# Kernel tuning notes

Measured on AMD Instinct MI355X. Metric: run time of the kernel, lower is better.

Reference implementation:

```python
import jax, jax.numpy as jnp
import numpy as np
from jax import lax

RATIOS = [0.5, 1.0, 2.0]
SCALES = [8, 16, 32]
BASE = 16
FEAT_STRIDE = 16
NMS_THRESH = 0.7
PRE_NMS = 2000
POST_NMS = 300
MIN_SIZE = 16.0
SCALE = 1.0
A = len(RATIOS) * len(SCALES)  # 9


def _anchor_base():
    ab = []
    py = px = BASE / 2.0
    for r in RATIOS:
        for s in SCALES:
            h = BASE * s * np.sqrt(r)
            w = BASE * s * np.sqrt(1.0 / r)
            ab.append([py - h / 2.0, px - w / 2.0, py + h / 2.0, px + w / 2.0])
    return jnp.asarray(np.array(ab, dtype=np.float32))  # (A,4)


def _shifted_anchors(H, W):
    base = _anchor_base()
    sy = jnp.arange(H, dtype=jnp.float32) * FEAT_STRIDE
    sx = jnp.arange(W, dtype=jnp.float32) * FEAT_STRIDE
    gy, gx = jnp.meshgrid(sy, sx, indexing='ij')
    shift = jnp.stack([gy.ravel(), gx.ravel(), gy.ravel(), gx.ravel()], axis=1)  # (K,4)
    return (shift[:, None, :] + base[None, :, :]).reshape(-1, 4)  # (K*A,4)


def _conv(x, w, b, pad):
    y = lax.conv_general_dilated(x, w, (1, 1), ((pad, pad), (pad, pad)),
                                 dimension_numbers=('NCHW', 'OIHW', 'NCHW'))
    return y + b[None, :, None, None]


def _loc2bbox(anchor, loc):
    h = anchor[:, 2] - anchor[:, 0]
    w = anchor[:, 3] - anchor[:, 1]
    cy = anchor[:, 0] + 0.5 * h
    cx = anchor[:, 1] + 0.5 * w
    dy, dx, dh, dw = loc[:, 0], loc[:, 1], loc[:, 2], loc[:, 3]
    ncy = dy * h + cy
    ncx = dx * w + cx
    nh = jnp.exp(dh) * h
    nw = jnp.exp(dw) * w
    return jnp.stack([ncy - 0.5 * nh, ncx - 0.5 * nw, ncy + 0.5 * nh, ncx + 0.5 * nw], axis=1)


def _iou_matrix(b):
    area = (b[:, 2] - b[:, 0]) * (b[:, 3] - b[:, 1])
    ty = jnp.maximum(b[:, None, 0], b[None, :, 0])
    tx = jnp.maximum(b[:, None, 1], b[None, :, 1])
    by = jnp.minimum(b[:, None, 2], b[None, :, 2])
    bx = jnp.minimum(b[:, None, 3], b[None, :, 3])
    inter = jnp.maximum(by - ty, 0.0) * jnp.maximum(bx - tx, 0.0)
    return inter / (area[:, None] + area[None, :] - inter)


def _proposals(loc_i, fg_i, anchor, img_h, img_w):
    boxes = _loc2bbox(anchor, loc_i)
    boxes = jnp.stack([
        jnp.clip(boxes[:, 0], 0.0, float(img_h)),
        jnp.clip(boxes[:, 1], 0.0, float(img_w)),
        jnp.clip(boxes[:, 2], 0.0, float(img_h)),
        jnp.clip(boxes[:, 3], 0.0, float(img_w)),
    ], axis=1)
    hs = boxes[:, 2] - boxes[:, 0]
    ws = boxes[:, 3] - boxes[:, 1]
    valid = (hs >= MIN_SIZE * SCALE) & (ws >= MIN_SIZE * SCALE)
    sc = jnp.where(valid, fg_i, -jnp.inf)
    top_sc, idx = lax.top_k(sc, PRE_NMS)          # sorted by score desc
    b = boxes[idx]                                # (PRE_NMS,4)
    iou = _iou_matrix(b)                          # (PRE_NMS,PRE_NMS)
    rng = jnp.arange(PRE_NMS)

    def body(i, keep):
        sup = (iou[i] > NMS_THRESH) & keep[i] & (rng > i)
        return keep & ~sup

    keep = lax.fori_loop(0, PRE_NMS, body, top_sc > -jnp.inf)
    order = jnp.argsort(jnp.where(keep, rng, PRE_NMS))  # kept indices first, score order
    sel = order[:POST_NMS]
    n_keep = jnp.sum(keep)
    valid_out = jnp.arange(POST_NMS) < n_keep
    rois = jnp.where(valid_out[:, None], b[sel], 0.0)
    return rois, valid_out


def setup_inputs() -> dict:
    key = jax.random.key(0)
    ks = jax.random.split(key, 4)
    return {
        'x': jax.random.normal(ks[0], (4, 1024, 64, 64), dtype=jnp.float32),
        'conv1_w': 0.01 * jax.random.normal(ks[1], (512, 1024, 3, 3), dtype=jnp.float32),
        'conv1_b': jnp.zeros((512,), dtype=jnp.float32),
        'score_w': 0.01 * jax.random.normal(ks[2], (18, 512, 1, 1), dtype=jnp.float32),
        'score_b': jnp.zeros((18,), dtype=jnp.float32),
        'loc_w': 0.01 * jax.random.normal(ks[3], (36, 512, 1, 1), dtype=jnp.float32),
        'loc_b': jnp.zeros((36,), dtype=jnp.float32),
        'img_h': 1024,
        'img_w': 1024,
    }


def reference(x, conv1_w, conv1_b, score_w, score_b, loc_w, loc_b, img_h, img_w):
    n, _, H, W = x.shape
    anchor = _shifted_anchors(H, W)                       # (HWA,4)
    mid = jax.nn.relu(_conv(x, conv1_w, conv1_b, 1))
    rpn_locs = _conv(mid, loc_w, loc_b, 0).transpose(0, 2, 3, 1).reshape(n, -1, 4)
    rpn_scores = _conv(mid, score_w, score_b, 0).transpose(0, 2, 3, 1)
    soft = jax.nn.softmax(rpn_scores.reshape(n, H, W, A, 2), axis=4)
    rpn_fg = soft[..., 1].reshape(n, -1)
    rpn_scores = rpn_scores.reshape(n, -1, 2)
    rois, valid = jax.vmap(lambda l, s: _proposals(l, s, anchor, img_h, img_w))(rpn_locs, rpn_fg)
    roi_indices = jnp.where(valid, jnp.arange(n, dtype=jnp.int32)[:, None], -1)
    return (rpn_locs, rpn_scores, rois.reshape(-1, 4), roi_indices.reshape(-1), anchor)
```

## Files before the change

### kernel.cpp

```cpp
#include <hip/hip_runtime.h>
#include <math.h>

#define NIMG 4
#define CIN 1024
#define CMID 512
#define HGT 64
#define WID 64
#define NA 9
#define NPOS 36864
#define PRE 2000
#define POST 300

#define LOCOFF   0
#define SCOREOFF 589824
#define ROISOFF  884736
#define RIDXOFF  889536
#define ANCHOFF  890736

__global__ __launch_bounds__(256) void wtrans_kernel(
    const float* __restrict__ w, float* __restrict__ wt)
{
    __shared__ float ts[64][65];
    const int t = threadIdx.x;
    const int rt0 = blockIdx.x * 64;
    const int ct0 = blockIdx.y * 64;
    const int j = t & 63;
    const int i0 = t >> 6;
#pragma unroll
    for (int k = 0; k < 16; ++k) {
        int i = i0 + k * 4;
        ts[i][j] = w[(size_t)(ct0 + i) * (CIN * 9) + rt0 + j];
    }
    __syncthreads();
#pragma unroll
    for (int k = 0; k < 16; ++k) {
        int jj = i0 + k * 4;
        wt[(size_t)(rt0 + jj) * CMID + ct0 + j] = ts[j][jj];
    }
}

__global__ __launch_bounds__(256) void conv1_kernel(
    const float* __restrict__ x, const float* __restrict__ wt,
    const float* __restrict__ bias, float* __restrict__ mid)
{
    __shared__ __align__(16) double xs[4][6][68];
    __shared__ __align__(16) double wsh[4][9][32];
    const int t = threadIdx.x;
    const int rowgrp = blockIdx.x, coutgrp = blockIdx.y, img = blockIdx.z;
    const int r0 = rowgrp * 4, c0 = coutgrp * 32;
    const int pixgrp = t & 7, cgrp = (t >> 3) & 7, rowi = t >> 6;
    const int p0 = pixgrp * 8, cc0 = cgrp * 4;

    double acc[8][4];
#pragma unroll
    for (int i = 0; i < 8; ++i)
#pragma unroll
        for (int c = 0; c < 4; ++c) acc[i][c] = 0.0;

    for (int ci0 = 0; ci0 < CIN; ci0 += 4) {
        for (int idx = t; idx < 4 * 6 * 66; idx += 256) {
            int cin = idx / 396, rem = idx % 396;
            int row = rem / 66, col = rem % 66;
            int gr = r0 - 1 + row, gc = col - 1;
            float v = 0.f;
            if (gr >= 0 && gr < HGT && gc >= 0 && gc < WID)
                v = x[((img * CIN + ci0 + cin) * HGT + gr) * WID + gc];
            xs[cin][row][col] = (double)v;
        }
        for (int idx = t; idx < 4 * 9 * 32; idx += 256) {
            int cout = idx & 31, r = idx >> 5;
            wsh[r / 9][r % 9][cout] =
                (double)wt[(size_t)((ci0 + r / 9) * 9 + r % 9) * CMID + c0 + cout];
        }
        __syncthreads();

#pragma unroll 1
        for (int cin = 0; cin < 4; ++cin) {
#pragma unroll
            for (int dy = 0; dy < 3; ++dy) {
                const double* xr = &xs[cin][rowi + dy][p0];
                double2 a0 = *(const double2*)(xr);
                double2 a1 = *(const double2*)(xr + 2);
                double2 a2 = *(const double2*)(xr + 4);
                double2 a3 = *(const double2*)(xr + 6);
                double2 a4 = *(const double2*)(xr + 8);
                double xd[10];
                xd[0] = a0.x; xd[1] = a0.y; xd[2] = a1.x; xd[3] = a1.y;
                xd[4] = a2.x; xd[5] = a2.y; xd[6] = a3.x; xd[7] = a3.y;
                xd[8] = a4.x; xd[9] = a4.y;
#pragma unroll
                for (int dx = 0; dx < 3; ++dx) {
                    const double* wp = &wsh[cin][dy * 3 + dx][cc0];
                    double2 wa = *(const double2*)(wp);
                    double2 wb = *(const double2*)(wp + 2);
#pragma unroll
                    for (int i = 0; i < 8; ++i) {
                        double xv = xd[i + dx];
                        acc[i][0] += xv * wa.x;
                        acc[i][1] += xv * wa.y;
                        acc[i][2] += xv * wb.x;
                        acc[i][3] += xv * wb.y;
                    }
                }
            }
        }
        __syncthreads();
    }

#pragma unroll
    for (int co = 0; co < 4; ++co) {
        double bb = (double)bias[c0 + cc0 + co];
        float tmp[8];
#pragma unroll
        for (int i = 0; i < 8; ++i) {
            double v = acc[i][co] + bb;
            v = v > 0.0 ? v : 0.0;
            tmp[i] = (float)v;
        }
        float* dst = &mid[((img * CMID + c0 + cc0 + co) * HGT + (r0 + rowi)) * WID + p0];
        *(float4*)dst = make_float4(tmp[0], tmp[1], tmp[2], tmp[3]);
        *(float4*)(dst + 4) = make_float4(tmp[4], tmp[5], tmp[6], tmp[7]);
    }
}

__global__ __launch_bounds__(256) void conv1x1_kernel(
    const float* __restrict__ mid,
    const float* __restrict__ sw, const float* __restrict__ sb,
    const float* __restrict__ lw, const float* __restrict__ lb,
    float* __restrict__ out, double* __restrict__ locws, double* __restrict__ keyws)
{
    const int t = threadIdx.x;
    const int p = blockIdx.x * 256 + t;
    const int g = blockIdx.y;
    const int img = blockIdx.z;

    double acc[14];
#pragma unroll
    for (int k = 0; k < 14; ++k) acc[k] = 0.0;

    const float* mp = &mid[(size_t)img * CMID * 4096 + p];
    for (int cin = 0; cin < CMID; ++cin) {
        double xd = (double)mp[(size_t)cin * 4096];
#pragma unroll
        for (int k = 0; k < 14; ++k) {
            int c = g * 14 + k;
            double wv = 0.0;
            if (c < 36)      wv = (double)lw[c * CMID + cin];
            else if (c < 54) wv = (double)sw[(c - 36) * CMID + cin];
            acc[k] += xd * wv;
        }
    }

    double prev = 0.0;
#pragma unroll
    for (int k = 0; k < 14; ++k) {
        int c = g * 14 + k;
        if (c >= 54) continue;
        if (c < 36) {
            double v = acc[k] + (double)lb[c];
            int a = c >> 2, cc = c & 3;
            size_t ix = (size_t)img * NPOS + (size_t)p * NA + a;
            locws[ix * 4 + cc] = v;
            out[LOCOFF + ix * 4 + cc] = (float)v;
        } else {
            int sc = c - 36;
            double v = acc[k] + (double)sb[sc];
            int a = sc >> 1;
            size_t ix = (size_t)img * NPOS + (size_t)p * NA + a;
            out[SCOREOFF + ix * 2 + (sc & 1)] = (float)v;
            if (sc & 1) keyws[ix] = v - prev;
            prev = v;
        }
    }
}

__device__ __forceinline__ unsigned mono_of(double k) {
    unsigned fb = __float_as_uint((float)k);
    return (fb & 0x80000000u) ? ~fb : (fb | 0x80000000u);
}

__global__ __launch_bounds__(256) void boxes_kernel(
    double* __restrict__ keyio, const double* __restrict__ locws,
    const int* __restrict__ imh, const int* __restrict__ imw,
    float* __restrict__ out, double* __restrict__ boxes, unsigned* __restrict__ hist)
{
    __shared__ unsigned lh[4096];
    const int t = threadIdx.x;
    const int img = blockIdx.y;
    const int pos = blockIdx.x * 256 + t;
    for (int i = t; i < 4096; i += 256) lh[i] = 0;
    __syncthreads();

    int a = pos % 9, hw = pos / 9;
    int hy = hw >> 6, hx = hw & 63;
    int r_idx = a / 3, s_idx = a % 3;
    double ratio = r_idx == 0 ? 0.5 : (r_idx == 1 ? 1.0 : 2.0);
    double scl   = s_idx == 0 ? 8.0 : (s_idx == 1 ? 16.0 : 32.0);
    double hh2 = 8.0 * scl * sqrt(ratio);
    double ww2 = 8.0 * scl * sqrt(1.0 / ratio);
    float ay1 = (float)(8.0 - hh2), ax1 = (float)(8.0 - ww2);
    float ay2 = (float)(8.0 + hh2), ax2 = (float)(8.0 + ww2);
    float sy = (float)(hy * 16), sx = (float)(hx * 16);
    float A0 = sy + ay1, A1 = sx + ax1, A2 = sy + ay2, A3 = sx + ax2;
    if (img == 0) {
        size_t ao = ANCHOFF + (size_t)pos * 4;
        out[ao + 0] = A0; out[ao + 1] = A1; out[ao + 2] = A2; out[ao + 3] = A3;
    }

    size_t ix = (size_t)img * NPOS + pos;
    const double* lp = &locws[ix * 4];
    double h = (double)A2 - (double)A0, w_ = (double)A3 - (double)A1;
    double cy = (double)A0 + 0.5 * h, cx = (double)A1 + 0.5 * w_;
    double dy = lp[0], dx = lp[1], dh = lp[2], dw = lp[3];
    double ncy = dy * h + cy, ncx = dx * w_ + cx;
    double nh = exp(dh) * h, nw = exp(dw) * w_;
    double Hc = (double)imh[0], Wc = (double)imw[0];
    double y1 = ncy - 0.5 * nh, x1 = ncx - 0.5 * nw;
    double y2 = ncy + 0.5 * nh, x2 = ncx + 0.5 * nw;
    y1 = fmin(fmax(y1, 0.0), Hc); x1 = fmin(fmax(x1, 0.0), Wc);
    y2 = fmin(fmax(y2, 0.0), Hc); x2 = fmin(fmax(x2, 0.0), Wc);
    boxes[ix * 4 + 0] = y1; boxes[ix * 4 + 1] = x1;
    boxes[ix * 4 + 2] = y2; boxes[ix * 4 + 3] = x2;

    bool valid = ((y2 - y1) >= 16.0) && ((x2 - x1) >= 16.0);
    double kg = valid ? keyio[ix] : -INFINITY;
    keyio[ix] = kg;
    atomicAdd(&lh[mono_of(kg) >> 20], 1u);
    __syncthreads();
    for (int i = t; i < 4096; i += 256)
        if (lh[i]) atomicAdd(&hist[img * 4096 + i], lh[i]);
}

__global__ void cutoff_kernel(const unsigned* __restrict__ hist, int* __restrict__ cutoffb)
{
    if (threadIdx.x) return;
    int img = blockIdx.x;
    unsigned cum = 0; int cb = 0;
    for (int b = 4095; b >= 0; --b) {
        cum += hist[img * 4096 + b];
        if (cum >= PRE) { cb = b; break; }
    }
    cutoffb[img] = cb;
}

__global__ __launch_bounds__(256) void compact_kernel(
    const double* __restrict__ keyio, const int* __restrict__ cutoffb,
    int* __restrict__ candCnt, int* __restrict__ candIdx, double* __restrict__ candKey)
{
    int img = blockIdx.y;
    int pos = blockIdx.x * 256 + threadIdx.x;
    size_t ix = (size_t)img * NPOS + pos;
    double k = keyio[ix];
    if ((int)(mono_of(k) >> 20) >= cutoffb[img]) {
        int p = atomicAdd(&candCnt[img], 1);
        candIdx[img * NPOS + p] = pos;
        candKey[(size_t)img * NPOS + p] = k;
    }
}

__global__ __launch_bounds__(256) void rank_kernel(
    const int* __restrict__ candCnt, const int* __restrict__ candIdx,
    const double* __restrict__ candKey, const double* __restrict__ boxes,
    int* __restrict__ topIdx, int* __restrict__ topValid, double* __restrict__ bsel)
{
    __shared__ double sk[256];
    __shared__ int si[256];
    int img = blockIdx.y, t = threadIdx.x;
    int M = candCnt[img];
    if (blockIdx.x * 256 >= M) return;
    int i = blockIdx.x * 256 + t;
    bool act = i < M;
    double ki = 0.0; int pi = 0;
    if (act) { ki = candKey[(size_t)img * NPOS + i]; pi = candIdx[img * NPOS + i]; }
    int rank = 0;
    for (int jb = 0; jb < M; jb += 256) {
        int j = jb + t;
        if (j < M) { sk[t] = candKey[(size_t)img * NPOS + j]; si[t] = candIdx[img * NPOS + j]; }
        __syncthreads();
        int lim = min(256, M - jb);
        if (act) {
            for (int jj = 0; jj < lim; ++jj) {
                double kj = sk[jj]; int pj = si[jj];
                rank += (kj > ki || (kj == ki && pj < pi)) ? 1 : 0;
            }
        }
        __syncthreads();
    }
    if (act && rank < PRE) {
        topIdx[img * PRE + rank] = pi;
        topValid[img * PRE + rank] = (ki != -INFINITY) ? 1 : 0;
        const double* bp = &boxes[((size_t)img * NPOS + pi) * 4];
        double* bs = &bsel[((size_t)img * PRE + rank) * 4];
        bs[0] = bp[0]; bs[1] = bp[1]; bs[2] = bp[2]; bs[3] = bp[3];
    }
}

__global__ __launch_bounds__(256) void mask_kernel(
    const double* __restrict__ bsel, unsigned long long* __restrict__ mask)
{
    int i = blockIdx.x, img = blockIdx.y, t = threadIdx.x;
    const double* bi = &bsel[((size_t)img * PRE + i) * 4];
    double y1i = bi[0], x1i = bi[1], y2i = bi[2], x2i = bi[3];
    double ai = (y2i - y1i) * (x2i - x1i);
#pragma unroll 1
    for (int it = 0; it < 8; ++it) {
        int j = it * 256 + t;
        bool pred = false;
        if (j < PRE && j > i) {
            const double* bj = &bsel[((size_t)img * PRE + j) * 4];
            double ty = fmax(y1i, bj[0]), tx = fmax(x1i, bj[1]);
            double by = fmin(y2i, bj[2]), bx = fmin(x2i, bj[3]);
            double inter = fmax(by - ty, 0.0) * fmax(bx - tx, 0.0);
            double aj = (bj[2] - bj[0]) * (bj[3] - bj[1]);
            double iou = inter / (ai + aj - inter);
            pred = iou > 0.7;
        }
        unsigned long long m = __ballot(pred);
        if ((t & 63) == 0)
            mask[((size_t)img * PRE + i) * 32 + it * 4 + (t >> 6)] = m;
    }
}

__global__ void nms_kernel(const unsigned long long* __restrict__ mask,
                           const int* __restrict__ topValid, int* __restrict__ keepA)
{
    int img = blockIdx.x, lane = threadIdx.x;
    size_t base = (size_t)img * PRE;
    unsigned long long remv = 0;
    if (lane < 32) {
        unsigned long long tv = 0;
        for (int b = 0; b < 64; ++b) {
            int idx = lane * 64 + b;
            if (idx < PRE && topValid[base + idx]) tv |= (1ull << b);
        }
        remv = ~tv;
    }
    const unsigned long long* mrow = &mask[base * 32];
    unsigned long long c0 = 0, c1 = 0, c2 = 0, c3 = 0;
    if (lane < 32) {
        c0 = mrow[(size_t)0 * 32 + lane]; c1 = mrow[(size_t)1 * 32 + lane];
        c2 = mrow[(size_t)2 * 32 + lane]; c3 = mrow[(size_t)3 * 32 + lane];
    }
    for (int i = 0; i < PRE; i += 4) {
        unsigned long long n0 = 0, n1 = 0, n2 = 0, n3 = 0;
        if (lane < 32 && i + 4 < PRE) {
            n0 = mrow[(size_t)(i + 4) * 32 + lane];
            n1 = mrow[(size_t)(i + 5) * 32 + lane];
            n2 = mrow[(size_t)(i + 6) * 32 + lane];
            n3 = mrow[(size_t)(i + 7) * 32 + lane];
        }
        {
            unsigned long long rw = __shfl(remv, i >> 6);
            int kp = !((rw >> (i & 63)) & 1ull);
            if (lane == 0) keepA[base + i] = kp;
            if (kp) remv |= c0;
        }
        {
            int ii = i + 1;
            unsigned long long rw = __shfl(remv, ii >> 6);
            int kp = !((rw >> (ii & 63)) & 1ull);
            if (lane == 0) keepA[base + ii] = kp;
            if (kp) remv |= c1;
        }
        {
            int ii = i + 2;
            unsigned long long rw = __shfl(remv, ii >> 6);
            int kp = !((rw >> (ii & 63)) & 1ull);
            if (lane == 0) keepA[base + ii] = kp;
            if (kp) remv |= c2;
        }
        {
            int ii = i + 3;
            unsigned long long rw = __shfl(remv, ii >> 6);
            int kp = !((rw >> (ii & 63)) & 1ull);
            if (lane == 0) keepA[base + ii] = kp;
            if (kp) remv |= c3;
        }
        c0 = n0; c1 = n1; c2 = n2; c3 = n3;
    }
}

__global__ __launch_bounds__(256) void final_kernel(
    const int* __restrict__ keepA, const double* __restrict__ bsel, float* __restrict__ out)
{
    __shared__ int ssum[256];
    __shared__ int stot;
    int img = blockIdx.x, t = threadIdx.x;
    size_t base = (size_t)img * PRE;
    int loc[8]; int s = 0;
#pragma unroll
    for (int k = 0; k < 8; ++k) {
        int i = t * 8 + k;
        loc[k] = (i < PRE) ? keepA[base + i] : 0;
        s += loc[k];
    }
    ssum[t] = s;
    __syncthreads();
    if (t == 0) {
        int run = 0;
        for (int u = 0; u < 256; ++u) { int tmp = ssum[u]; ssum[u] = run; run += tmp; }
        stot = run;
    }
    __syncthreads();
    int run = ssum[t];
#pragma unroll
    for (int k = 0; k < 8; ++k) {
        int i = t * 8 + k;
        if (i < PRE && loc[k]) {
            int p = run++;
            if (p < POST) {
                const double* bp = &bsel[(base + i) * 4];
                size_t ro = ROISOFF + ((size_t)img * POST + p) * 4;
                out[ro + 0] = (float)bp[0]; out[ro + 1] = (float)bp[1];
                out[ro + 2] = (float)bp[2]; out[ro + 3] = (float)bp[3];
                out[RIDXOFF + img * POST + p] = (float)img;
            }
        }
    }
    __syncthreads();
    int nk = stot;
    for (int r = t; r < POST; r += 256) {
        if (r >= nk) {
            size_t ro = ROISOFF + ((size_t)img * POST + r) * 4;
            out[ro + 0] = 0.f; out[ro + 1] = 0.f; out[ro + 2] = 0.f; out[ro + 3] = 0.f;
            out[RIDXOFF + img * POST + r] = -1.f;
        }
    }
}

extern "C" void kernel_launch(void* const* d_in, const int* in_sizes, int n_in,
                              void* d_out, int out_size, void* d_ws, size_t ws_size,
                              hipStream_t stream)
{
    const float* x   = (const float*)d_in[0];
    const float* c1w = (const float*)d_in[1];
    const float* c1b = (const float*)d_in[2];
    const float* sw  = (const float*)d_in[3];
    const float* sb  = (const float*)d_in[4];
    const float* lw  = (const float*)d_in[5];
    const float* lb  = (const float*)d_in[6];
    const int*   ih  = (const int*)d_in[7];
    const int*   iw  = (const int*)d_in[8];
    float* out = (float*)d_out;
    (void)in_sizes; (void)n_in; (void)out_size; (void)ws_size;

    char* ws = (char*)d_ws;
    size_t off = 0;
    auto alloc = [&](size_t bytes) -> void* {
        void* p = (void*)(ws + off);
        off = (off + bytes + 255) & ~(size_t)255;
        return p;
    };
    float*  mid      = (float*) alloc((size_t)NIMG * CMID * 4096 * 4);
    float*  wtr      = (float*) alloc((size_t)CMID * CIN * 9 * 4);
    double* locws    = (double*)alloc((size_t)NIMG * NPOS * 4 * 8);
    double* keyws    = (double*)alloc((size_t)NIMG * NPOS * 8);
    double* boxes    = (double*)alloc((size_t)NIMG * NPOS * 4 * 8);
    unsigned* hist   = (unsigned*)alloc((size_t)NIMG * 4096 * 4);
    int*    cutoffb  = (int*)   alloc(64);
    int*    candCnt  = (int*)   alloc(64);
    int*    candIdx  = (int*)   alloc((size_t)NIMG * NPOS * 4);
    double* candKey  = (double*)alloc((size_t)NIMG * NPOS * 8);
    int*    topIdx   = (int*)   alloc((size_t)NIMG * PRE * 4);
    int*    topValid = (int*)   alloc((size_t)NIMG * PRE * 4);
    double* bsel     = (double*)alloc((size_t)NIMG * PRE * 4 * 8);
    unsigned long long* mask = (unsigned long long*)alloc((size_t)NIMG * PRE * 32 * 8);
    int*    keepA    = (int*)   alloc((size_t)NIMG * PRE * 4);

    hipMemsetAsync(hist, 0, (size_t)NIMG * 4096 * 4, stream);
    hipMemsetAsync(candCnt, 0, 64, stream);

    wtrans_kernel <<<dim3(144, 8),       256, 0, stream>>>(c1w, wtr);
    conv1_kernel  <<<dim3(16, 16, NIMG), 256, 0, stream>>>(x, wtr, c1b, mid);
    conv1x1_kernel<<<dim3(16, 4, NIMG),  256, 0, stream>>>(mid, sw, sb, lw, lb, out, locws, keyws);
    boxes_kernel  <<<dim3(144, NIMG),    256, 0, stream>>>(keyws, locws, ih, iw, out, boxes, hist);
    cutoff_kernel <<<NIMG, 64, 0, stream>>>(hist, cutoffb);
    compact_kernel<<<dim3(144, NIMG),    256, 0, stream>>>(keyws, cutoffb, candCnt, candIdx, candKey);
    rank_kernel   <<<dim3(144, NIMG),    256, 0, stream>>>(candCnt, candIdx, candKey, boxes,
                                                           topIdx, topValid, bsel);
    mask_kernel   <<<dim3(PRE, NIMG),    256, 0, stream>>>(bsel, mask);
    nms_kernel    <<<NIMG, 64, 0, stream>>>(mask, topValid, keepA);
    final_kernel  <<<NIMG, 256, 0, stream>>>(keepA, bsel, out);
}
```

Before: 4.748 ms.

## Retile FP64 conv1 to two rows per thread with register-prefetched input

The 3x3 conv kernel now gives each thread two output rows, so each loaded input row and weight value is reused across both rows and adjacent dy taps. Input staging doubles to 8 channels per step and is kept as float in LDS, converted to double on read. The next chunk is prefetched from global memory into registers while the current one computes. It also sets a minimum of 2 blocks per SM and halves the grid. The cost is more registers (64 double accumulators plus 21 prefetch floats), which could cause spills or lower occupancy, and fewer blocks (512) to fill the GPU.

```diff
diff --git a/kernel.cpp b/kernel.cpp
--- a/kernel.cpp
+++ b/kernel.cpp
@@ -39,87 +39,123 @@
     }
 }
 
-__global__ __launch_bounds__(256) void conv1_kernel(
+#define NXS (8 * 10 * 66)
+#define XPRE 21
+
+__global__ __launch_bounds__(256, 2) void conv1_kernel(
     const float* __restrict__ x, const float* __restrict__ wt,
     const float* __restrict__ bias, float* __restrict__ mid)
 {
-    __shared__ __align__(16) double xs[4][6][68];
-    __shared__ __align__(16) double wsh[4][9][32];
+    __shared__ float  Xl[8][10][67];
+    __shared__ double Wl[8][9][32];
     const int t = threadIdx.x;
-    const int rowgrp = blockIdx.x, coutgrp = blockIdx.y, img = blockIdx.z;
-    const int r0 = rowgrp * 4, c0 = coutgrp * 32;
-    const int pixgrp = t & 7, cgrp = (t >> 3) & 7, rowi = t >> 6;
-    const int p0 = pixgrp * 8, cc0 = cgrp * 4;
-
-    double acc[8][4];
-#pragma unroll
-    for (int i = 0; i < 8; ++i)
-#pragma unroll
-        for (int c = 0; c < 4; ++c) acc[i][c] = 0.0;
-
-    for (int ci0 = 0; ci0 < CIN; ci0 += 4) {
-        for (int idx = t; idx < 4 * 6 * 66; idx += 256) {
-            int cin = idx / 396, rem = idx % 396;
-            int row = rem / 66, col = rem % 66;
-            int gr = r0 - 1 + row, gc = col - 1;
-            float v = 0.f;
-            if (gr >= 0 && gr < HGT && gc >= 0 && gc < WID)
-                v = x[((img * CIN + ci0 + cin) * HGT + gr) * WID + gc];
-            xs[cin][row][col] = (double)v;
-        }
-        for (int idx = t; idx < 4 * 9 * 32; idx += 256) {
-            int cout = idx & 31, r = idx >> 5;
-            wsh[r / 9][r % 9][cout] =
-                (double)wt[(size_t)((ci0 + r / 9) * 9 + r % 9) * CMID + c0 + cout];
+    const int rowblk = blockIdx.x, coutblk = blockIdx.y, img = blockIdx.z;
+    const int y0 = rowblk * 8, cout0 = coutblk * 32;
+    const int pg = t & 7, cg = (t >> 3) & 7, rp = t >> 6;
+    const int p0 = pg * 8, cc0 = cg * 4, rp2 = rp * 2;
+
+    double acc[2][8][4];
+#pragma unroll
+    for (int rr = 0; rr < 2; ++rr)
+#pragma unroll
+        for (int i = 0; i < 8; ++i)
+#pragma unroll
+            for (int c = 0; c < 4; ++c) acc[rr][i][c] = 0.0;
+
+    float xpre[XPRE];
+
+#define XLOAD(CI0)                                                        \
+    {                                                                     \
+        _Pragma("unroll")                                                 \
+        for (int k = 0; k < XPRE; ++k) {                                  \
+            int idx = t + k * 256;                                        \
+            float v = 0.f;                                                \
+            if (idx < NXS) {                                              \
+                int cin = idx / 660, rem = idx % 660;                     \
+                int row = rem / 66, col = rem % 66;                       \
+                int gr = y0 - 1 + row, gc = col - 1;                      \
+                if (gr >= 0 && gr < HGT && gc >= 0 && gc < WID)           \
+                    v = x[((img * CIN + (CI0) + cin) * HGT + gr) * WID + gc]; \
+            }                                                             \
+            xpre[k] = v;                                                  \
+        }                                                                 \
+    }
+
+    XLOAD(0)
+
+#pragma unroll 1
+    for (int s = 0; s < 128; ++s) {
+        const int ci0 = s * 8;
+#pragma unroll
+        for (int k = 0; k < XPRE; ++k) {
+            int idx = t + k * 256;
+            if (idx < NXS) {
+                int cin = idx / 660, rem = idx % 660;
+                int row = rem / 66, col = rem % 66;
+                Xl[cin][row][col] = xpre[k];
+            }
+        }
+#pragma unroll
+        for (int k = 0; k < 9; ++k) {
+            int idx = t + k * 256;
+            int r = idx >> 5, cl = idx & 31;
+            Wl[r / 9][r % 9][cl] =
+                (double)wt[(size_t)((ci0 + r / 9) * 9 + (r % 9)) * CMID + cout0 + cl];
         }
         __syncthreads();
 
+        if (s + 1 < 128) XLOAD(ci0 + 8)
+
+#define LOADROW(DST, CIN, LROW)                                           \
+        _Pragma("unroll")                                                 \
+        for (int j = 0; j < 10; ++j)                                      \
+            DST[j] = (double)Xl[CIN][LROW][p0 + j];
+
+#define TAP(CIN, DY, RA, RB)                                              \
+        _Pragma("unroll")                                                 \
+        for (int dx = 0; dx < 3; ++dx) {                                  \
+            const double* wp = &Wl[CIN][(DY) * 3 + dx][cc0];              \
+            double w0 = wp[0], w1 = wp[1], w2 = wp[2], w3 = wp[3];        \
+            _Pragma("unroll")                                             \
+            for (int i = 0; i < 8; ++i) {                                 \
+                double xa = RA[i + dx], xb = RB[i + dx];                  \
+                acc[0][i][0] += xa * w0; acc[0][i][1] += xa * w1;         \
+                acc[0][i][2] += xa * w2; acc[0][i][3] += xa * w3;         \
+                acc[1][i][0] += xb * w0; acc[1][i][1] += xb * w1;         \
+                acc[1][i][2] += xb * w2; acc[1][i][3] += xb * w3;         \
+            }                                                             \
+        }
+
 #pragma unroll 1
-        for (int cin = 0; cin < 4; ++cin) {
-#pragma unroll
-            for (int dy = 0; dy < 3; ++dy) {
-                const double* xr = &xs[cin][rowi + dy][p0];
-                double2 a0 = *(const double2*)(xr);
-                double2 a1 = *(const double2*)(xr + 2);
-                double2 a2 = *(const double2*)(xr + 4);
-                double2 a3 = *(const double2*)(xr + 6);
-                double2 a4 = *(const double2*)(xr + 8);
-                double xd[10];
-                xd[0] = a0.x; xd[1] = a0.y; xd[2] = a1.x; xd[3] = a1.y;
-                xd[4] = a2.x; xd[5] = a2.y; xd[6] = a3.x; xd[7] = a3.y;
-                xd[8] = a4.x; xd[9] = a4.y;
-#pragma unroll
-                for (int dx = 0; dx < 3; ++dx) {
-                    const double* wp = &wsh[cin][dy * 3 + dx][cc0];
-                    double2 wa = *(const double2*)(wp);
-                    double2 wb = *(const double2*)(wp + 2);
-#pragma unroll
-                    for (int i = 0; i < 8; ++i) {
-                        double xv = xd[i + dx];
-                        acc[i][0] += xv * wa.x;
-                        acc[i][1] += xv * wa.y;
-                        acc[i][2] += xv * wb.x;
-                        acc[i][3] += xv * wb.y;
-                    }
-                }
+        for (int cin = 0; cin < 8; ++cin) {
+            double r0d[10], r1d[10], r2d[10], r3d[10];
+            LOADROW(r0d, cin, rp2 + 0)
+            LOADROW(r1d, cin, rp2 + 1)
+            TAP(cin, 0, r0d, r1d)
+            LOADROW(r2d, cin, rp2 + 2)
+            TAP(cin, 1, r1d, r2d)
+            LOADROW(r3d, cin, rp2 + 3)
+            TAP(cin, 2, r2d, r3d)
+        }
+        __syncthreads();
+    }
+
+#pragma unroll
+    for (int rr = 0; rr < 2; ++rr) {
+#pragma unroll
+        for (int co = 0; co < 4; ++co) {
+            double bb = (double)bias[cout0 + cc0 + co];
+            float tmp[8];
+#pragma unroll
+            for (int i = 0; i < 8; ++i) {
+                double v = acc[rr][i][co] + bb;
+                v = v > 0.0 ? v : 0.0;
+                tmp[i] = (float)v;
             }
-        }
-        __syncthreads();
-    }
-
-#pragma unroll
-    for (int co = 0; co < 4; ++co) {
-        double bb = (double)bias[c0 + cc0 + co];
-        float tmp[8];
-#pragma unroll
-        for (int i = 0; i < 8; ++i) {
-            double v = acc[i][co] + bb;
-            v = v > 0.0 ? v : 0.0;
-            tmp[i] = (float)v;
-        }
-        float* dst = &mid[((img * CMID + c0 + cc0 + co) * HGT + (r0 + rowi)) * WID + p0];
-        *(float4*)dst = make_float4(tmp[0], tmp[1], tmp[2], tmp[3]);
-        *(float4*)(dst + 4) = make_float4(tmp[4], tmp[5], tmp[6], tmp[7]);
+            float* dst = &mid[((img * CMID + cout0 + cc0 + co) * HGT + (y0 + rp2 + rr)) * WID + p0];
+            *(float4*)dst = make_float4(tmp[0], tmp[1], tmp[2], tmp[3]);
+            *(float4*)(dst + 4) = make_float4(tmp[4], tmp[5], tmp[6], tmp[7]);
+        }
     }
 }
 
@@ -471,7 +507,7 @@
     hipMemsetAsync(candCnt, 0, 64, stream);
 
     wtrans_kernel <<<dim3(144, 8),       256, 0, stream>>>(c1w, wtr);
-    conv1_kernel  <<<dim3(16, 16, NIMG), 256, 0, stream>>>(x, wtr, c1b, mid);
+    conv1_kernel  <<<dim3(8, 16, NIMG),  256, 0, stream>>>(x, wtr, c1b, mid);
     conv1x1_kernel<<<dim3(16, 4, NIMG),  256, 0, stream>>>(mid, sw, sb, lw, lb, out, locws, keyws);
     boxes_kernel  <<<dim3(144, NIMG),    256, 0, stream>>>(keyws, locws, ih, iw, out, boxes, hist);
     cutoff_kernel <<<NIMG, 64, 0, stream>>>(hist, cutoffb);
```

Result: slower. 6.042 ms (+27.3%).
